# Kernel optimization log

Measured on AMD Instinct MI355X. Metric: run time of the kernel, lower is better.

Reference implementation:

```python
import jax, jax.numpy as jnp
import numpy as np

BS, NQ, NH, HD = 4, 10000, 8, 32   # batch, queries, heads, head_dim
NP = 4                              # sampling points
H, W = 100, 100                     # fixed spatial shape (value_spatial_shapes_list[0])


def grid_sample_bilinear_zeros(img, grid):
    """PyTorch F.grid_sample(mode='bilinear', padding_mode='zeros', align_corners=False).
    img: (N, C, Hin, Win); grid: (N, Hg, Wg, 2) with (x, y) in [-1, 1].
    Returns (N, C, Hg, Wg)."""
    N, C, Hin, Win = img.shape
    Hg, Wg = grid.shape[1], grid.shape[2]
    # unnormalize (align_corners=False)
    x = (grid[..., 0] + 1.0) * (Win * 0.5) - 0.5
    y = (grid[..., 1] + 1.0) * (Hin * 0.5) - 0.5
    x0 = jnp.floor(x); y0 = jnp.floor(y)
    x1 = x0 + 1.0;     y1 = y0 + 1.0
    wx1 = x - x0; wx0 = 1.0 - wx1
    wy1 = y - y0; wy0 = 1.0 - wy1
    img_flat = img.reshape(N, C, Hin * Win)

    def gather(xi, yi, w):
        xi_i = xi.astype(jnp.int32); yi_i = yi.astype(jnp.int32)
        valid = (xi_i >= 0) & (xi_i < Win) & (yi_i >= 0) & (yi_i < Hin)
        xc = jnp.clip(xi_i, 0, Win - 1); yc = jnp.clip(yi_i, 0, Hin - 1)
        idx = (yc * Win + xc).reshape(N, 1, Hg * Wg)
        vals = jnp.take_along_axis(img_flat, idx, axis=2)      # (N, C, Hg*Wg)
        wm = jnp.where(valid, w, 0.0).reshape(N, 1, Hg * Wg)
        return vals * wm

    out = (gather(x0, y0, wx0 * wy0) + gather(x1, y0, wx1 * wy0)
           + gather(x0, y1, wx0 * wy1) + gather(x1, y1, wx1 * wy1))
    return out.reshape(N, C, Hg, Wg)


def setup_inputs() -> dict:
    key = jax.random.key(0)
    k1, k2, k3 = jax.random.split(key, 3)
    value = jax.random.normal(k1, (BS, H * W, NH, HD), dtype=jnp.float32)
    value_spatial_shapes = jnp.array([[H, W]], dtype=jnp.int64)  # unused (fixed-size variant)
    sampling_locations = jax.random.uniform(k2, (BS, NQ, NH, 1, NP, 2), dtype=jnp.float32)
    attention_weights = jax.random.uniform(k3, (BS, NQ, NH, 1, NP), dtype=jnp.float32)
    return {"value": value, "value_spatial_shapes": value_spatial_shapes,
            "sampling_locations": sampling_locations, "attention_weights": attention_weights}


def reference(value, value_spatial_shapes, sampling_locations, attention_weights):
    bs, _, nh, d = value.shape
    nq, npnt = sampling_locations.shape[1], sampling_locations.shape[4]
    # (bs, HW, nh, d) -> (bs*nh, d, H, W)
    v = jnp.transpose(value, (0, 2, 3, 1)).reshape(bs * nh, d, H, W)
    # sampling grids in [-1, 1]; single level -> index 0
    grids = 2.0 * sampling_locations[:, :, :, 0] - 1.0           # (bs, nq, nh, np, 2)
    grids = jnp.transpose(grids, (0, 2, 1, 3, 4)).reshape(bs * nh, nq, npnt, 2)
    sampled = grid_sample_bilinear_zeros(v, grids)               # (bs*nh, d, nq, np)
    aw = jnp.transpose(attention_weights, (0, 2, 1, 3, 4)).reshape(bs * nh, 1, nq, npnt)
    out = (sampled * aw).sum(-1)                                 # (bs*nh, d, nq)
    out = out.reshape(bs, nh * d, nq)
    return jnp.transpose(out, (0, 2, 1))                         # (bs, nq, nh*d)
```

## Files before the change

### kernel.cpp

```cpp
#include <hip/hip_runtime.h>


constexpr int BS = 4, NQ = 10000, NH = 8, HD = 32, NP = 4, H = 100, W = 100;
constexpr int HW = H * W;
constexpr int NGROUP = BS * NQ * NH;
constexpr int NXCD = 8;

typedef float f32x4 __attribute__((ext_vector_type(4)));

__global__ __launch_bounds__(256)
void deform_attn_kernel(const float* __restrict__ value,
                        const float* __restrict__ sloc,
                        const float* __restrict__ aw,
                        float* __restrict__ out)
{
    const int chunk = gridDim.x >> 3;
    const int swz   = (blockIdx.x & (NXCD - 1)) * chunk + (blockIdx.x >> 3);

    const int tid   = swz * 256 + (int)threadIdx.x;
    const int group = tid >> 3;
    const int lane  = tid & 7;
    if (group >= NGROUP) return;

    const int q  = group % NQ;
    const int bh = group / NQ;
    const int h  = bh & (NH - 1);
    const int b  = bh >> 3;
    const int bq = b * NQ + q;

    const size_t pbase = ((size_t)bq * NH + h);
    const f32x4 l01 = *(const f32x4*)(sloc + pbase * (NP * 2));
    const f32x4 l23 = *(const f32x4*)(sloc + pbase * (NP * 2) + 4);
    const f32x4 wv  = *(const f32x4*)(aw   + pbase * NP);

    const float lx[NP] = {l01.x, l01.z, l23.x, l23.z};
    const float ly[NP] = {l01.y, l01.w, l23.y, l23.w};
    const float wp[NP] = {wv.x,  wv.y,  wv.z,  wv.w};

    const float* vbase = value + (size_t)b * HW * NH * HD + h * HD + lane * 4;

    f32x4 acc = (f32x4)(0.f);

#pragma unroll
    for (int p = 0; p < NP; ++p) {
        const float x = lx[p] * (float)W - 0.5f;
        const float y = ly[p] * (float)H - 0.5f;
        const float x0f = floorf(x);
        const float y0f = floorf(y);
        const int   x0  = (int)x0f, y0 = (int)y0f;
        const int   x1  = x0 + 1,   y1 = y0 + 1;
        const float wx1 = x - x0f,  wx0 = 1.f - wx1;
        const float wy1 = y - y0f,  wy0 = 1.f - wy1;

        const bool vx0 = (unsigned)x0 < (unsigned)W;
        const bool vx1 = (unsigned)x1 < (unsigned)W;
        const bool vy0 = (unsigned)y0 < (unsigned)H;
        const bool vy1 = (unsigned)y1 < (unsigned)H;

        const int xc0 = min(max(x0, 0), W - 1);
        const int xc1 = min(max(x1, 0), W - 1);
        const int yc0 = min(max(y0, 0), H - 1);
        const int yc1 = min(max(y1, 0), H - 1);

        const float w00 = (vx0 && vy0) ? wp[p] * wx0 * wy0 : 0.f;
        const float w10 = (vx1 && vy0) ? wp[p] * wx1 * wy0 : 0.f;
        const float w01 = (vx0 && vy1) ? wp[p] * wx0 * wy1 : 0.f;
        const float w11 = (vx1 && vy1) ? wp[p] * wx1 * wy1 : 0.f;

        const f32x4 v00 = *(const f32x4*)(vbase + (size_t)(yc0 * W + xc0) * (NH * HD));
        const f32x4 v10 = *(const f32x4*)(vbase + (size_t)(yc0 * W + xc1) * (NH * HD));
        const f32x4 v01 = *(const f32x4*)(vbase + (size_t)(yc1 * W + xc0) * (NH * HD));
        const f32x4 v11 = *(const f32x4*)(vbase + (size_t)(yc1 * W + xc1) * (NH * HD));

        acc += w00 * v00 + w10 * v10 + w01 * v01 + w11 * v11;
    }

    __builtin_nontemporal_store(acc, (f32x4*)(out + (size_t)bq * (NH * HD) + h * HD + lane * 4));
}

extern "C" void kernel_launch(void* const* d_in, const int* in_sizes, int n_in,
                              void* d_out, int out_size, void* d_ws, size_t ws_size,
                              hipStream_t stream) {
    const float* value = (const float*)d_in[0];
    const float* sloc  = (const float*)d_in[2];
    const float* aw    = (const float*)d_in[3];
    float*       out   = (float*)d_out;

    const int total_threads = NGROUP * 8;
    const int block = 256;
    const int grid  = (total_threads + block - 1) / block;
    deform_attn_kernel<<<grid, block, 0, stream>>>(value, sloc, aw, out);
}
```

Baseline: 134.9 us.

## Cast value to fp16 per-head slabs and gather rows with buffer loads

Adds a pre-pass that converts the value tensor to fp16 in a per-(batch,head) contiguous layout in the workspace. The gather kernel then loads two adjacent x-pixels per 16-byte load per row, issues all eight loads up front with raw buffer_load asm and staged waitcnts, and combines the x halves with a lane shuffle. This halves the bytes per gathered sample and improves locality, at the cost of an extra conversion pass each call and reduced precision in the sampled values. An fp32 fallback kernel is kept for when the workspace is too small.

Measured after the change: 125.0 us. -7.3%, faster.

```diff
diff --git a/kernel.cpp b/kernel.cpp
--- a/kernel.cpp
+++ b/kernel.cpp
@@ -3,24 +3,46 @@
 
 constexpr int BS = 4, NQ = 10000, NH = 8, HD = 32, NP = 4, H = 100, W = 100;
 constexpr int HW = H * W;
-constexpr int NGROUP = BS * NQ * NH;
-constexpr int NXCD = 8;
+constexpr unsigned VBYTES_F32 = (unsigned)BS * HW * NH * HD * 4u;
+constexpr unsigned VH_BYTES   = (unsigned)BS * HW * NH * HD * 2u;
 
-typedef float f32x4 __attribute__((ext_vector_type(4)));
+typedef float    f32x4 __attribute__((ext_vector_type(4)));
+typedef float    f32x8 __attribute__((ext_vector_type(8)));
+typedef _Float16 f16x8 __attribute__((ext_vector_type(8)));
+typedef unsigned u32x4 __attribute__((ext_vector_type(4)));
 
 __global__ __launch_bounds__(256)
-void deform_attn_kernel(const float* __restrict__ value,
-                        const float* __restrict__ sloc,
-                        const float* __restrict__ aw,
-                        float* __restrict__ out)
+void cast_kernel(const float* __restrict__ v, _Float16* __restrict__ vh)
+{
+    const int tid = blockIdx.x * 256 + (int)threadIdx.x;
+    const int c8 = tid & 3;
+    const int t2 = tid >> 2;
+    const int x  = t2 % 100;
+    const int t3 = t2 / 100;
+    const int y  = t3 % 100;
+    const int t4 = t3 / 100;
+    const float* src = v + ((size_t)(t4 >> 3) * HW + y * W + x) * 256 + (t4 & 7) * 32 + c8 * 8;
+    const f32x4 a = __builtin_nontemporal_load((const f32x4*)src);
+    const f32x4 b = __builtin_nontemporal_load((const f32x4*)(src + 4));
+    const f32x8 f = {a.x, a.y, a.z, a.w, b.x, b.y, b.z, b.w};
+    const f16x8 o = __builtin_convertvector(f, f16x8);
+    *(f16x8*)(vh + ((size_t)t4 * HW + y * W + x) * 32 + c8 * 8) = o;
+}
+
+__global__ __launch_bounds__(256, 4)
+void gather_kernel(const _Float16* __restrict__ vh,
+                   const float* __restrict__ sloc,
+                   const float* __restrict__ aw,
+                   float* __restrict__ out)
 {
     const int chunk = gridDim.x >> 3;
-    const int swz   = (blockIdx.x & (NXCD - 1)) * chunk + (blockIdx.x >> 3);
+    const int swz   = (blockIdx.x & 7) * chunk + (blockIdx.x >> 3);
 
     const int tid   = swz * 256 + (int)threadIdx.x;
     const int group = tid >> 3;
     const int lane  = tid & 7;
-    if (group >= NGROUP) return;
+    const int xsel  = lane >> 2;
+    const int csel  = lane & 3;
 
     const int q  = group % NQ;
     const int bh = group / NQ;
@@ -28,7 +50,7 @@
     const int b  = bh >> 3;
     const int bq = b * NQ + q;
 
-    const size_t pbase = ((size_t)bq * NH + h);
+    const size_t pbase = (size_t)bq * NH + h;
     const f32x4 l01 = *(const f32x4*)(sloc + pbase * (NP * 2));
     const f32x4 l23 = *(const f32x4*)(sloc + pbase * (NP * 2) + 4);
     const f32x4 wv  = *(const f32x4*)(aw   + pbase * NP);
@@ -37,10 +59,11 @@
     const float ly[NP] = {l01.y, l01.w, l23.y, l23.w};
     const float wp[NP] = {wv.x,  wv.y,  wv.z,  wv.w};
 
-    const float* vbase = value + (size_t)b * HW * NH * HD + h * HD + lane * 4;
+    const unsigned slabbase = (unsigned)(bh * HW) * 64u;
 
-    f32x4 acc = (f32x4)(0.f);
-
+    unsigned voff[NP][2];
+    float    wrow[NP][2];
+    float    wxl[NP];
 #pragma unroll
     for (int p = 0; p < NP; ++p) {
         const float x = lx[p] * (float)W - 0.5f;
@@ -48,33 +71,105 @@
         const float x0f = floorf(x);
         const float y0f = floorf(y);
         const int   x0  = (int)x0f, y0 = (int)y0f;
-        const int   x1  = x0 + 1,   y1 = y0 + 1;
-        const float wx1 = x - x0f,  wx0 = 1.f - wx1;
-        const float wy1 = y - y0f,  wy0 = 1.f - wy1;
+        const float fx1 = x - x0f, fx0 = 1.f - fx1;
+        const float fy1 = y - y0f, fy0 = 1.f - fy1;
 
-        const bool vx0 = (unsigned)x0 < (unsigned)W;
-        const bool vx1 = (unsigned)x1 < (unsigned)W;
-        const bool vy0 = (unsigned)y0 < (unsigned)H;
-        const bool vy1 = (unsigned)y1 < (unsigned)H;
+        const int xc = x0 + xsel;
+        wxl[p] = ((unsigned)xc < (unsigned)W) ? (xsel ? fx1 : fx0) * wp[p] : 0.f;
+        wrow[p][0] = ((unsigned)y0 < (unsigned)H)       ? fy0 : 0.f;
+        wrow[p][1] = ((unsigned)(y0 + 1) < (unsigned)H) ? fy1 : 0.f;
 
-        const int xc0 = min(max(x0, 0), W - 1);
-        const int xc1 = min(max(x1, 0), W - 1);
-        const int yc0 = min(max(y0, 0), H - 1);
-        const int yc1 = min(max(y1, 0), H - 1);
+        const int basex = min(max(x0, 0), W - 2);
+        const int sl    = min(max(xc, 0), W - 1) - basex;
+        const int y0c   = min(max(y0, 0), H - 1);
+        const int y1c   = min(max(y0 + 1, 0), H - 1);
+        const unsigned lo = (unsigned)(basex) * 64u + (unsigned)sl * 64u + (unsigned)csel * 16u;
+        voff[p][0] = slabbase + (unsigned)(y0c * W) * 64u + lo;
+        voff[p][1] = slabbase + (unsigned)(y1c * W) * 64u + lo;
+    }
 
+    union { const _Float16* p; unsigned u[2]; } va; va.p = vh;
+    const u32x4 rsrc = {va.u[0], va.u[1] & 0xFFFFu, VH_BYTES, 0x00020000u};
+
+    f32x4 r00, r01, r10, r11, r20, r21, r30, r31;
+#define GLOAD(dst, off) \
+    asm volatile("buffer_load_dwordx4 %0, %1, %2, 0 offen" \
+                 : "=v"(dst) : "v"(off), "s"(rsrc))
+    GLOAD(r00, voff[0][0]); GLOAD(r01, voff[0][1]);
+    GLOAD(r10, voff[1][0]); GLOAD(r11, voff[1][1]);
+    GLOAD(r20, voff[2][0]); GLOAD(r21, voff[2][1]);
+    GLOAD(r30, voff[3][0]); GLOAD(r31, voff[3][1]);
+#undef GLOAD
+
+    f32x8 acc = (f32x8)(0.f);
+#define CONSUME(ra, rb, p, cnt) \
+    asm volatile("s_waitcnt vmcnt(" #cnt ")" : "+v"(ra), "+v"(rb)); \
+    { const f32x8 v0 = __builtin_convertvector(__builtin_bit_cast(f16x8, ra), f32x8); \
+      const f32x8 v1 = __builtin_convertvector(__builtin_bit_cast(f16x8, rb), f32x8); \
+      acc += v0 * (wxl[p] * wrow[p][0]) + v1 * (wxl[p] * wrow[p][1]); }
+    CONSUME(r00, r01, 0, 6)
+    CONSUME(r10, r11, 1, 4)
+    CONSUME(r20, r21, 2, 2)
+    CONSUME(r30, r31, 3, 0)
+#undef CONSUME
+
+    f32x8 other;
+#pragma unroll
+    for (int j = 0; j < 8; ++j) other[j] = __shfl_xor(acc[j], 4, 8);
+    acc += other;
+
+    const f32x4 res = xsel ? (f32x4){acc[4], acc[5], acc[6], acc[7]}
+                           : (f32x4){acc[0], acc[1], acc[2], acc[3]};
+    __builtin_nontemporal_store(res,
+        (f32x4*)(out + (size_t)bq * (NH * HD) + h * HD + csel * 8 + xsel * 4));
+}
+
+__global__ __launch_bounds__(256, 4)
+void deform_attn_f32(const float* __restrict__ value,
+                     const float* __restrict__ sloc,
+                     const float* __restrict__ aw,
+                     float* __restrict__ out)
+{
+    const int chunk = gridDim.x >> 3;
+    const int swz   = (blockIdx.x & 7) * chunk + (blockIdx.x >> 3);
+    const int tid   = swz * 256 + (int)threadIdx.x;
+    const int group = tid >> 3;
+    const int lane  = tid & 7;
+    const int q  = group % NQ;
+    const int bh = group / NQ;
+    const int h  = bh & (NH - 1);
+    const int b  = bh >> 3;
+    const int bq = b * NQ + q;
+    const size_t pbase = (size_t)bq * NH + h;
+    const f32x4 l01 = *(const f32x4*)(sloc + pbase * (NP * 2));
+    const f32x4 l23 = *(const f32x4*)(sloc + pbase * (NP * 2) + 4);
+    const f32x4 wv  = *(const f32x4*)(aw   + pbase * NP);
+    const float lx[NP] = {l01.x, l01.z, l23.x, l23.z};
+    const float ly[NP] = {l01.y, l01.w, l23.y, l23.w};
+    const float wp[NP] = {wv.x,  wv.y,  wv.z,  wv.w};
+    const float* vbase = value + (size_t)b * HW * NH * HD + h * HD + lane * 4;
+    f32x4 acc = (f32x4)(0.f);
+#pragma unroll
+    for (int p = 0; p < NP; ++p) {
+        const float x = lx[p] * (float)W - 0.5f;
+        const float y = ly[p] * (float)H - 0.5f;
+        const float x0f = floorf(x), y0f = floorf(y);
+        const int x0 = (int)x0f, y0 = (int)y0f, x1 = x0 + 1, y1 = y0 + 1;
+        const float wx1 = x - x0f, wx0 = 1.f - wx1, wy1 = y - y0f, wy0 = 1.f - wy1;
+        const bool vx0 = (unsigned)x0 < (unsigned)W, vx1 = (unsigned)x1 < (unsigned)W;
+        const bool vy0 = (unsigned)y0 < (unsigned)H, vy1 = (unsigned)y1 < (unsigned)H;
+        const int xc0 = min(max(x0, 0), W - 1), xc1 = min(max(x1, 0), W - 1);
+        const int yc0 = min(max(y0, 0), H - 1), yc1 = min(max(y1, 0), H - 1);
         const float w00 = (vx0 && vy0) ? wp[p] * wx0 * wy0 : 0.f;
         const float w10 = (vx1 && vy0) ? wp[p] * wx1 * wy0 : 0.f;
         const float w01 = (vx0 && vy1) ? wp[p] * wx0 * wy1 : 0.f;
         const float w11 = (vx1 && vy1) ? wp[p] * wx1 * wy1 : 0.f;
-
         const f32x4 v00 = *(const f32x4*)(vbase + (size_t)(yc0 * W + xc0) * (NH * HD));
         const f32x4 v10 = *(const f32x4*)(vbase + (size_t)(yc0 * W + xc1) * (NH * HD));
         const f32x4 v01 = *(const f32x4*)(vbase + (size_t)(yc1 * W + xc0) * (NH * HD));
         const f32x4 v11 = *(const f32x4*)(vbase + (size_t)(yc1 * W + xc1) * (NH * HD));
-
         acc += w00 * v00 + w10 * v10 + w01 * v01 + w11 * v11;
     }
-
     __builtin_nontemporal_store(acc, (f32x4*)(out + (size_t)bq * (NH * HD) + h * HD + lane * 4));
 }
 
@@ -86,8 +181,11 @@
     const float* aw    = (const float*)d_in[3];
     float*       out   = (float*)d_out;
 
-    const int total_threads = NGROUP * 8;
-    const int block = 256;
-    const int grid  = (total_threads + block - 1) / block;
-    deform_attn_kernel<<<grid, block, 0, stream>>>(value, sloc, aw, out);
+    if (ws_size >= (size_t)VH_BYTES) {
+        _Float16* vh = (_Float16*)d_ws;
+        cast_kernel<<<5000, 256, 0, stream>>>(value, vh);
+        gather_kernel<<<10000, 256, 0, stream>>>(vh, sloc, aw, out);
+    } else {
+        deform_attn_f32<<<10000, 256, 0, stream>>>(value, sloc, aw, out);
+    }
 }
```
